# Performance work log

Measured on AMD Instinct MI355X. Metric: run time of the kernel, lower is better.

Reference implementation:

```python
import jax, jax.numpy as jnp
import numpy as np

HEADS = 16
MAX_DIST = 1024

def setup_inputs() -> dict:
    key = jax.random.key(0)
    k1, k2, k3, k4 = jax.random.split(key, 4)
    b, n, dim = 2, 2048, 1024
    x = jax.random.normal(k1, (b, n, dim), dtype=jnp.float32)
    W_qkv = jax.random.normal(k2, (3 * dim, dim), dtype=jnp.float32) * (dim ** -0.5)
    W_out = jax.random.normal(k3, (dim, dim), dtype=jnp.float32) * (dim ** -0.5)
    b_out = jnp.zeros((dim,), dtype=jnp.float32)
    rel_emb = jax.random.normal(k4, (2 * MAX_DIST + 1, HEADS), dtype=jnp.float32) * 0.02
    return {"x": x, "W_qkv": W_qkv, "W_out": W_out, "b_out": b_out, "rel_emb": rel_emb}

def reference(x, W_qkv, W_out, b_out, rel_emb):
    b, n, dim = x.shape
    h = HEADS
    d = dim // h
    scale = d ** -0.5
    qkv = jnp.einsum('bnd,ed->bne', x, W_qkv)  # [b, n, 3*dim]
    q, k, v = jnp.split(qkv, 3, axis=-1)
    def to_heads(t):
        return t.reshape(b, n, h, d).transpose(0, 2, 1, 3)  # b h n d
    q, k, v = to_heads(q), to_heads(k), to_heads(v)
    # relative position bias: [1, h, n, n]
    dist = jnp.arange(n)[None, :] - jnp.arange(n)[:, None]
    idx = jnp.clip(dist, -MAX_DIST, MAX_DIST) + MAX_DIST  # [n, n]
    rel_bias = rel_emb[idx].transpose(2, 0, 1)[None]  # [1, h, n, n]
    scores = jnp.einsum('bhqd,bhkd->bhqk', q, k) * scale + rel_bias
    attn = jax.nn.softmax(scores, axis=-1)
    out = jnp.einsum('bhqk,bhkd->bhqd', attn, v)
    out = out.transpose(0, 2, 1, 3).reshape(b, n, dim)
    return jnp.einsum('bnd,ed->bne', out, W_out) + b_out
```

## Files before the change

### kernel.cpp

```cpp
#include <hip/hip_runtime.h>
#include <hip/hip_bf16.h>

typedef __attribute__((ext_vector_type(8))) short short8;
typedef __attribute__((ext_vector_type(4))) float f32x4;
typedef __attribute__((ext_vector_type(16))) float f32x16;
typedef float f32x4u __attribute__((ext_vector_type(4), aligned(4)));
typedef __attribute__((ext_vector_type(4))) unsigned short u16x4;
typedef __attribute__((ext_vector_type(2))) unsigned int u32x2;
typedef __attribute__((ext_vector_type(4))) unsigned int u32x4;
typedef __hip_bfloat16 bf16;

#define SCALE_Q 0.18033688f

#define GLD_LDS16(g, l) __builtin_amdgcn_global_load_lds(                      \
    (const __attribute__((address_space(1))) void*)(g),                        \
    (__attribute__((address_space(3))) void*)(l), 16, 0, 0)

static __device__ __forceinline__ f32x4 mfma16(short8 a, short8 b, f32x4 c) {
  return __builtin_amdgcn_mfma_f32_16x16x32_bf16(a, b, c, 0, 0, 0);
}
static __device__ __forceinline__ f32x16 mfma32(short8 a, short8 b, f32x16 c) {
  return __builtin_amdgcn_mfma_f32_32x32x16_bf16(a, b, c, 0, 0, 0);
}

static __device__ __forceinline__ unsigned cvtpk(float lo, float hi) {
  unsigned r;
  asm("v_cvt_pk_bf16_f32 %0, %1, %2" : "=v"(r) : "v"(lo), "v"(hi));
  return r;
}

static __device__ __forceinline__ float fexp2(float x) {
  float r;
  asm("v_exp_f32 %0, %1" : "=v"(r) : "v"(x));
  return r;
}

static __device__ __forceinline__ float bf2f(unsigned short u) {
  return __builtin_bit_cast(float, (unsigned)u << 16);
}

#define PLSWAP(a, b) asm("v_permlane32_swap_b32 %0, %1" : "+v"(a), "+v"(b))

__global__ __launch_bounds__(256) void k_pre(
    const float* __restrict__ x, const float* __restrict__ Wqkv,
    const float* __restrict__ Wout, const float* __restrict__ rel,
    bf16* __restrict__ xb, bf16* __restrict__ wqb, bf16* __restrict__ wob,
    float* __restrict__ relpf) {
  int bid = blockIdx.x;
  if (bid < 4096) {
    const float* in;
    bf16* out;
    long i;
    if (bid < 2048) {
      in = x; out = xb; i = (long)bid * 256 + threadIdx.x;
    } else if (bid < 3584) {
      in = Wqkv; out = wqb; i = (long)(bid - 2048) * 256 + threadIdx.x;
    } else {
      in = Wout; out = wob; i = (long)(bid - 3584) * 256 + threadIdx.x;
    }
    f32x4 v0 = *(const f32x4*)(in + i * 8);
    f32x4 v1 = *(const f32x4*)(in + i * 8 + 4);
    u32x4 o;
    o[0] = cvtpk(v0[0], v0[1]);
    o[1] = cvtpk(v0[2], v0[3]);
    o[2] = cvtpk(v1[0], v1[1]);
    o[3] = cvtpk(v1[2], v1[3]);
    *(u32x4*)((unsigned short*)out + i * 8) = o;
  } else {
    int base = (bid - 4096) * 1024 + threadIdx.x;
#pragma unroll
    for (int k = 0; k < 4; ++k) {
      int i = base + k * 256;
      int h = i >> 12, ii = i & 4095;
      int dd = ii - 2047;
      dd = dd < -1024 ? -1024 : (dd > 1024 ? 1024 : dd);
      relpf[i] = rel[(size_t)(dd + 1024) * 16 + h] * 1.44269504f - 16.0f;
    }
  }
}

__global__ __launch_bounds__(256, 3) void k_gemm(
    const bf16* __restrict__ A, const bf16* __restrict__ B,
    int M, int N, int K, int epi,
    bf16* __restrict__ Qb, bf16* __restrict__ Kb, bf16* __restrict__ Vt,
    float* __restrict__ Out, const float* __restrict__ bias) {
  __shared__ bf16 lA[3][4096];
  __shared__ bf16 lB[3][4096];
  const int tid = threadIdx.x, w = tid >> 6, l = tid & 63;
  const int m0 = blockIdx.x * 128, n0 = blockIdx.y * 128;
  const int wrow = (w >> 1) * 64, wcol = (w & 1) * 64;
  const int fr = l & 15, fq = l >> 4;
  f32x4 acc[4][4] = {};
  const int c0 = w * 64 + l, c1 = c0 + 256;
  const bf16* Ag0 = A + (size_t)(m0 + (c0 >> 2)) * K + (c0 & 3) * 8;
  const bf16* Ag1 = A + (size_t)(m0 + (c1 >> 2)) * K + (c1 & 3) * 8;
  const bf16* Bg0 = B + (size_t)(n0 + (c0 >> 2)) * K + (c0 & 3) * 8;
  const bf16* Bg1 = B + (size_t)(n0 + (c1 >> 2)) * K + (c1 & 3) * 8;
  bf16* lA0 = &lA[0][w * 512];
  bf16* lA1 = &lA[0][2048 + w * 512];
  bf16* lB0 = &lB[0][w * 512];
  bf16* lB1 = &lB[0][2048 + w * 512];

#define GSTAGE(T, BI)                                                          \
  do {                                                                         \
    const int ko_ = (T) * 32;                                                  \
    GLD_LDS16(Ag0 + ko_, lA0 + (BI) * 4096);                                   \
    GLD_LDS16(Ag1 + ko_, lA1 + (BI) * 4096);                                   \
    GLD_LDS16(Bg0 + ko_, lB0 + (BI) * 4096);                                   \
    GLD_LDS16(Bg1 + ko_, lB1 + (BI) * 4096);                                   \
  } while (0)

  const int nk = K >> 5;
  GSTAGE(0, 0);
  __builtin_amdgcn_sched_barrier(0);
  GSTAGE(1, 1);
  __builtin_amdgcn_sched_barrier(0);

  int bc_ = 0, bs_ = 2;
  for (int t = 0; t < nk; ++t) {
    asm volatile("s_waitcnt vmcnt(4)" ::: "memory");
    __builtin_amdgcn_s_barrier();
    __builtin_amdgcn_sched_barrier(0);
    int tt = (t + 2 < nk) ? t + 2 : nk - 1;
    GSTAGE(tt, bs_);
    __builtin_amdgcn_sched_barrier(0);
    const bf16* pA = &lA[bc_][0];
    const bf16* pB = &lB[bc_][0];
    short8 af[4], bfv[4];
#pragma unroll
    for (int mi = 0; mi < 4; ++mi)
      af[mi] = *(const short8*)&pA[(wrow + mi * 16 + fr) * 32 + fq * 8];
#pragma unroll
    for (int ni = 0; ni < 4; ++ni)
      bfv[ni] = *(const short8*)&pB[(wcol + ni * 16 + fr) * 32 + fq * 8];
    __builtin_amdgcn_s_setprio(1);
#pragma unroll
    for (int mi = 0; mi < 4; ++mi)
#pragma unroll
      for (int ni = 0; ni < 4; ++ni)
        acc[mi][ni] = mfma16(bfv[ni], af[mi], acc[mi][ni]);
    __builtin_amdgcn_s_setprio(0);
    bc_ = (bc_ == 2) ? 0 : bc_ + 1;
    bs_ = (bs_ == 2) ? 0 : bs_ + 1;
  }
#undef GSTAGE

  if (epi == 0) {
#pragma unroll
    for (int mi = 0; mi < 4; ++mi)
#pragma unroll
      for (int ni = 0; ni < 4; ++ni) {
        int t = m0 + wrow + mi * 16 + fr;
        int e4 = n0 + wcol + ni * 16 + fq * 4;
        int sect = e4 >> 10, eh = (e4 >> 6) & 15, dh = e4 & 63;
        int b = t >> 11, tt = t & 2047;
        f32x4 a = acc[mi][ni];
        if (sect < 2) {
          size_t idx = (((size_t)b * 16 + eh) * 2048 + tt) * 64 + dh;
          float sc = (sect == 0) ? SCALE_Q : 1.f;
          u32x2 ov;
          ov[0] = cvtpk(a[0] * sc, a[1] * sc);
          ov[1] = cvtpk(a[2] * sc, a[3] * sc);
          bf16* dst = (sect == 0) ? Qb : Kb;
          *(u32x2*)(dst + idx) = ov;
        } else {
          size_t vb = ((size_t)((b << 4) + eh) * 64 + dh) * 2048 + tt;
          unsigned p0 = cvtpk(a[0], a[1]);
          unsigned p1 = cvtpk(a[2], a[3]);
          unsigned short* vp = (unsigned short*)Vt;
          vp[vb] = (unsigned short)p0;
          vp[vb + 2048] = (unsigned short)(p0 >> 16);
          vp[vb + 4096] = (unsigned short)p1;
          vp[vb + 6144] = (unsigned short)(p1 >> 16);
        }
      }
  } else {
#pragma unroll
    for (int mi = 0; mi < 4; ++mi)
#pragma unroll
      for (int ni = 0; ni < 4; ++ni) {
        int t = m0 + wrow + mi * 16 + fr;
        int e4 = n0 + wcol + ni * 16 + fq * 4;
        f32x4 bv = *(const f32x4*)(bias + e4);
        f32x4 a = acc[mi][ni];
        f32x4 o = {a[0] + bv[0], a[1] + bv[1], a[2] + bv[2], a[3] + bv[3]};
        *(f32x4*)(Out + (size_t)t * N + e4) = o;
      }
  }
}

__global__ __launch_bounds__(256, 2) void k_attn(
    const bf16* __restrict__ Qb, const bf16* __restrict__ Kb,
    const bf16* __restrict__ Vt, const float* __restrict__ relpf,
    bf16* __restrict__ AO) {
  __shared__ bf16 lK[2][2][4096];
  __shared__ bf16 lV[2][2][4096];

  const int id = blockIdx.x;
  const int xcd = id & 7, j = id >> 3;
  const int bh = xcd * 4 + (j >> 4), qt = j & 15;
  const int h = bh & 15, b = bh >> 4;
  const int tid = threadIdx.x, w = tid >> 6, l = tid & 63;
  const int r32 = l & 31, hl = l >> 5, rs7 = r32 & 7;
  const int qh = w & 1, kvh = w >> 1;
  const int kvb = kvh * 1024;
  const int q0 = qt * 128 + qh * 64;

  const bf16* Kbh = Kb + (size_t)bh * 2048 * 64;
  const bf16* Vbh = Vt + (size_t)bh * 64 * 2048;
  const int pl = tid & 127;
  const bf16* Ksp[4];
  const bf16* Vsp[4];
#pragma unroll
  for (int s = 0; s < 4; ++s) {
    int ck = pl + 128 * s;
    int kr = ck >> 3, kc = (ck & 7) ^ (kr & 7);
    Ksp[s] = Kbh + (size_t)kr * 64 + kc * 8;
    Vsp[s] = Vbh + (size_t)kr * 2048 + kc * 8;
  }

#define STAGE(KT, BI)                                                          \
  do {                                                                         \
    _Pragma("unroll") for (int s_ = 0; s_ < 4; ++s_) {                         \
      int ck_ = pl + 128 * s_;                                                 \
      GLD_LDS16(Ksp[s_] + (size_t)(KT) * 64, &lK[kvh][BI][ck_ * 8]);           \
      GLD_LDS16(Vsp[s_] + (KT), &lV[kvh][BI][ck_ * 8]);                        \
    }                                                                          \
  } while (0)

  const bf16* Qp = Qb + ((size_t)bh * 2048 + q0 + r32) * 64;
  short8 qf0[4], qf1[4];
#pragma unroll
  for (int ks = 0; ks < 4; ++ks) {
    qf0[ks] = *(const short8*)(Qp + ks * 16 + hl * 8);
    qf1[ks] = *(const short8*)(Qp + 32 * 64 + ks * 16 + hl * 8);
  }

  const float* bp0 = relpf + h * 4096 + (2047 + 4 * hl - q0 - r32);
  const float* bp1 = bp0 - 32;

  float ll0 = 0.f, ll1 = 0.f;
  f32x16 oa0 = {}, ob0 = {}, oa1 = {}, ob1 = {};

  STAGE(kvb, 0);
  __builtin_amdgcn_sched_barrier(0);

  int cur = 0;
  for (int t = 0; t < 16; ++t) {
    const int kt = kvb + t * 64;
    asm volatile("s_waitcnt vmcnt(0)" ::: "memory");
    __builtin_amdgcn_s_barrier();
    __builtin_amdgcn_sched_barrier(0);
    f32x16 sa[2], sb[2];
#pragma unroll
    for (int kb = 0; kb < 2; ++kb)
#pragma unroll
      for (int g = 0; g < 4; ++g) {
        f32x4u va = *(const f32x4u*)(bp0 + kt + kb * 32 + 8 * g);
        f32x4u vb = *(const f32x4u*)(bp1 + kt + kb * 32 + 8 * g);
#pragma unroll
        for (int e = 0; e < 4; ++e) {
          sa[kb][g * 4 + e] = va[e];
          sb[kb][g * 4 + e] = vb[e];
        }
      }
    __builtin_amdgcn_sched_barrier(0);
    if (t < 15) STAGE(kt + 64, cur ^ 1);
    __builtin_amdgcn_sched_barrier(0);
    const bf16* lKc = &lK[kvh][cur][0];
    const bf16* lVc = &lV[kvh][cur][0];
    __builtin_amdgcn_s_setprio(1);
#pragma unroll
    for (int kb = 0; kb < 2; ++kb)
#pragma unroll
      for (int ks = 0; ks < 4; ++ks) {
        short8 kf = *(const short8*)&lKc[(kb * 32 + r32) * 64 +
                                         (((2 * ks + hl) ^ rs7) * 8)];
        sa[kb] = mfma32(kf, qf0[ks], sa[kb]);
        sb[kb] = mfma32(kf, qf1[ks], sb[kb]);
      }
    __builtin_amdgcn_s_setprio(0);
    float ra[4] = {0.f, 0.f, 0.f, 0.f}, rb[4] = {0.f, 0.f, 0.f, 0.f};
#pragma unroll
    for (int kb = 0; kb < 2; ++kb)
#pragma unroll
      for (int reg = 0; reg < 16; ++reg) {
        sa[kb][reg] = fexp2(sa[kb][reg]);
        ra[reg & 3] += sa[kb][reg];
        sb[kb][reg] = fexp2(sb[kb][reg]);
        rb[reg & 3] += sb[kb][reg];
      }
    ll0 += (ra[0] + ra[1]) + (ra[2] + ra[3]);
    ll1 += (rb[0] + rb[1]) + (rb[2] + rb[3]);
#pragma unroll
    for (int kb = 0; kb < 2; ++kb) {
#pragma unroll
      for (int kh = 0; kh < 2; ++kh) {
        const int e = kh * 8;
        const int ks = kb * 2 + kh;
        const int cc = ((2 * ks + hl) ^ rs7) * 8;
        unsigned a0 = cvtpk(sa[kb][e + 0], sa[kb][e + 1]);
        unsigned a1 = cvtpk(sa[kb][e + 2], sa[kb][e + 3]);
        unsigned b0 = cvtpk(sa[kb][e + 4], sa[kb][e + 5]);
        unsigned b1 = cvtpk(sa[kb][e + 6], sa[kb][e + 7]);
        PLSWAP(a0, b0);
        PLSWAP(a1, b1);
        u32x4 pw0 = {a0, a1, b0, b1};
        short8 pf0 = __builtin_bit_cast(short8, pw0);
        unsigned c0 = cvtpk(sb[kb][e + 0], sb[kb][e + 1]);
        unsigned c1 = cvtpk(sb[kb][e + 2], sb[kb][e + 3]);
        unsigned d0 = cvtpk(sb[kb][e + 4], sb[kb][e + 5]);
        unsigned d1 = cvtpk(sb[kb][e + 6], sb[kb][e + 7]);
        PLSWAP(c0, d0);
        PLSWAP(c1, d1);
        u32x4 pw1 = {c0, c1, d0, d1};
        short8 pf1 = __builtin_bit_cast(short8, pw1);
        short8 v0 = *(const short8*)&lVc[r32 * 64 + cc];
        short8 v1 = *(const short8*)&lVc[(32 + r32) * 64 + cc];
        __builtin_amdgcn_s_setprio(1);
        oa0 = mfma32(v0, pf0, oa0);
        ob0 = mfma32(v1, pf0, ob0);
        oa1 = mfma32(v0, pf1, oa1);
        ob1 = mfma32(v1, pf1, ob1);
        __builtin_amdgcn_s_setprio(0);
      }
    }
    cur ^= 1;
  }
#undef STAGE

  float l0t = ll0 + __shfl_xor(ll0, 32);
  float l1t = ll1 + __shfl_xor(ll1, 32);
  __syncthreads();
  char* pbase = (qh == 0) ? (char*)&lK[0][0][0] : (char*)&lV[0][0][0];
  float* lf = (float*)(pbase + 64 * 136);
  unsigned* pw = (unsigned*)(pbase + l * 136);
  if (kvh == 1) {
#pragma unroll
    for (int k = 0; k < 8; ++k) {
      pw[k] = cvtpk(oa0[2 * k], oa0[2 * k + 1]);
      pw[8 + k] = cvtpk(ob0[2 * k], ob0[2 * k + 1]);
      pw[16 + k] = cvtpk(oa1[2 * k], oa1[2 * k + 1]);
      pw[24 + k] = cvtpk(ob1[2 * k], ob1[2 * k + 1]);
    }
    if (hl == 0) {
      lf[r32] = l0t;
      lf[32 + r32] = l1t;
    }
  }
  __syncthreads();
  if (kvh == 0) {
    float ls0 = l0t + lf[r32];
    float ls1 = l1t + lf[32 + r32];
#pragma unroll
    for (int k = 0; k < 8; ++k) {
      unsigned u;
      u = pw[k];
      oa0[2 * k] += bf2f((unsigned short)u);
      oa0[2 * k + 1] += bf2f((unsigned short)(u >> 16));
      u = pw[8 + k];
      ob0[2 * k] += bf2f((unsigned short)u);
      ob0[2 * k + 1] += bf2f((unsigned short)(u >> 16));
      u = pw[16 + k];
      oa1[2 * k] += bf2f((unsigned short)u);
      oa1[2 * k + 1] += bf2f((unsigned short)(u >> 16));
      u = pw[24 + k];
      ob1[2 * k] += bf2f((unsigned short)u);
      ob1[2 * k + 1] += bf2f((unsigned short)(u >> 16));
    }
    float rin0 = 1.f / ls0, rin1 = 1.f / ls1;
    bf16* aor = AO + ((size_t)(b * 2048 + q0 + r32)) * 1024 + h * 64 + hl * 4;
    bf16* ao1 = aor + (size_t)32 * 1024;
#pragma unroll
    for (int rg = 0; rg < 4; ++rg) {
      u32x2 ov;
      ov[0] = cvtpk(oa0[4 * rg + 0] * rin0, oa0[4 * rg + 1] * rin0);
      ov[1] = cvtpk(oa0[4 * rg + 2] * rin0, oa0[4 * rg + 3] * rin0);
      *(u32x2*)(aor + rg * 8) = ov;
      ov[0] = cvtpk(ob0[4 * rg + 0] * rin0, ob0[4 * rg + 1] * rin0);
      ov[1] = cvtpk(ob0[4 * rg + 2] * rin0, ob0[4 * rg + 3] * rin0);
      *(u32x2*)(aor + 32 + rg * 8) = ov;
      ov[0] = cvtpk(oa1[4 * rg + 0] * rin1, oa1[4 * rg + 1] * rin1);
      ov[1] = cvtpk(oa1[4 * rg + 2] * rin1, oa1[4 * rg + 3] * rin1);
      *(u32x2*)(ao1 + rg * 8) = ov;
      ov[0] = cvtpk(ob1[4 * rg + 0] * rin1, ob1[4 * rg + 1] * rin1);
      ov[1] = cvtpk(ob1[4 * rg + 2] * rin1, ob1[4 * rg + 3] * rin1);
      *(u32x2*)(ao1 + 32 + rg * 8) = ov;
    }
  }
}

extern "C" void kernel_launch(void* const* d_in, const int* in_sizes, int n_in,
                              void* d_out, int out_size, void* d_ws,
                              size_t ws_size, hipStream_t stream) {
  const float* x = (const float*)d_in[0];
  const float* Wqkv = (const float*)d_in[1];
  const float* Wout = (const float*)d_in[2];
  const float* bout = (const float*)d_in[3];
  const float* rel = (const float*)d_in[4];
  float* out = (float*)d_out;

  char* p = (char*)d_ws;
  bf16* xb  = (bf16*)(p);
  bf16* wqb = (bf16*)(p + (8ull << 20));
  bf16* wob = (bf16*)(p + (14ull << 20));
  bf16* Qb  = (bf16*)(p + (16ull << 20));
  bf16* Kb  = (bf16*)(p + (24ull << 20));
  bf16* Vtr = (bf16*)(p + (32ull << 20));
  bf16* aob = (bf16*)(p + (40ull << 20));
  float* relpf = (float*)(p + (48ull << 20));

  k_pre<<<4160, 256, 0, stream>>>(x, Wqkv, Wout, rel, xb, wqb, wob, relpf);
  k_gemm<<<dim3(32, 24), 256, 0, stream>>>(xb, wqb, 4096, 3072, 1024, 0,
                                           Qb, Kb, Vtr, nullptr, nullptr);
  k_attn<<<512, 256, 0, stream>>>(Qb, Kb, Vtr, relpf, aob);
  k_gemm<<<dim3(32, 8), 256, 0, stream>>>(aob, wob, 4096, 1024, 1024, 1,
                                          nullptr, nullptr, nullptr, out, bout);
}
```

Before: 119.0 us.

## Swizzle GEMM LDS layout and use narrower tiles for output projection

Applies an XOR swizzle to the 16-byte chunk index in the LDS tiles of the QKV GEMM, in both the global-to-LDS load addresses and the fragment reads, to reduce LDS bank conflicts. Adds a dedicated output-projection GEMM with 128x64 tiles, which doubles the grid from 256 to 512 blocks so more CUs are busy on the 4096x1024 problem. The cost is lower per-block reuse of A and a second, near-duplicate kernel to maintain.

```diff
diff --git a/kernel.cpp b/kernel.cpp
--- a/kernel.cpp
+++ b/kernel.cpp
@@ -92,10 +92,11 @@
   const int fr = l & 15, fq = l >> 4;
   f32x4 acc[4][4] = {};
   const int c0 = w * 64 + l, c1 = c0 + 256;
-  const bf16* Ag0 = A + (size_t)(m0 + (c0 >> 2)) * K + (c0 & 3) * 8;
-  const bf16* Ag1 = A + (size_t)(m0 + (c1 >> 2)) * K + (c1 & 3) * 8;
-  const bf16* Bg0 = B + (size_t)(n0 + (c0 >> 2)) * K + (c0 & 3) * 8;
-  const bf16* Bg1 = B + (size_t)(n0 + (c1 >> 2)) * K + (c1 & 3) * 8;
+  const int r0c = c0 >> 2, r1c = c1 >> 2;
+  const bf16* Ag0 = A + (size_t)(m0 + r0c) * K + ((c0 & 3) ^ (r0c & 3)) * 8;
+  const bf16* Ag1 = A + (size_t)(m0 + r1c) * K + ((c1 & 3) ^ (r1c & 3)) * 8;
+  const bf16* Bg0 = B + (size_t)(n0 + r0c) * K + ((c0 & 3) ^ (r0c & 3)) * 8;
+  const bf16* Bg1 = B + (size_t)(n0 + r1c) * K + ((c1 & 3) ^ (r1c & 3)) * 8;
   bf16* lA0 = &lA[0][w * 512];
   bf16* lA1 = &lA[0][2048 + w * 512];
   bf16* lB0 = &lB[0][w * 512];
@@ -128,11 +129,15 @@
     const bf16* pB = &lB[bc_][0];
     short8 af[4], bfv[4];
 #pragma unroll
-    for (int mi = 0; mi < 4; ++mi)
-      af[mi] = *(const short8*)&pA[(wrow + mi * 16 + fr) * 32 + fq * 8];
-#pragma unroll
-    for (int ni = 0; ni < 4; ++ni)
-      bfv[ni] = *(const short8*)&pB[(wcol + ni * 16 + fr) * 32 + fq * 8];
+    for (int mi = 0; mi < 4; ++mi) {
+      int ra = wrow + mi * 16 + fr;
+      af[mi] = *(const short8*)&pA[ra * 32 + ((fq ^ (ra & 3)) * 8)];
+    }
+#pragma unroll
+    for (int ni = 0; ni < 4; ++ni) {
+      int rb = wcol + ni * 16 + fr;
+      bfv[ni] = *(const short8*)&pB[rb * 32 + ((fq ^ (rb & 3)) * 8)];
+    }
     __builtin_amdgcn_s_setprio(1);
 #pragma unroll
     for (int mi = 0; mi < 4; ++mi)
@@ -187,6 +192,83 @@
         *(f32x4*)(Out + (size_t)t * N + e4) = o;
       }
   }
+}
+
+__global__ __launch_bounds__(256, 3) void k_gemm2(
+    const bf16* __restrict__ A, const bf16* __restrict__ B,
+    float* __restrict__ Out, const float* __restrict__ bias) {
+  __shared__ bf16 lA[3][4096];
+  __shared__ bf16 lB[3][2048];
+  const int K = 1024, N = 1024;
+  const int tid = threadIdx.x, w = tid >> 6, l = tid & 63;
+  const int m0 = blockIdx.x * 128, n0 = blockIdx.y * 64;
+  const int wrow = (w >> 1) * 64, wcol = (w & 1) * 32;
+  const int fr = l & 15, fq = l >> 4;
+  f32x4 acc[4][2] = {};
+  const int a0r = tid >> 2, a1r = (tid + 256) >> 2;
+  const bf16* Ag0 = A + (size_t)(m0 + a0r) * K + (((tid & 3) ^ (a0r & 3)) * 8);
+  const bf16* Ag1 = A + (size_t)(m0 + a1r) * K +
+                    ((((tid + 256) & 3) ^ (a1r & 3)) * 8);
+  const bf16* Bg0 = B + (size_t)(n0 + a0r) * K + (((tid & 3) ^ (a0r & 3)) * 8);
+
+#define G2STAGE(T, BI)                                                         \
+  do {                                                                         \
+    const int ko_ = (T) * 32;                                                  \
+    GLD_LDS16(Ag0 + ko_, &lA[BI][tid * 8]);                                    \
+    GLD_LDS16(Ag1 + ko_, &lA[BI][(tid + 256) * 8]);                            \
+    GLD_LDS16(Bg0 + ko_, &lB[BI][tid * 8]);                                    \
+  } while (0)
+
+  const int nk = K >> 5;
+  G2STAGE(0, 0);
+  __builtin_amdgcn_sched_barrier(0);
+  G2STAGE(1, 1);
+  __builtin_amdgcn_sched_barrier(0);
+
+  int bc_ = 0, bs_ = 2;
+  for (int t = 0; t < nk; ++t) {
+    asm volatile("s_waitcnt vmcnt(3)" ::: "memory");
+    __builtin_amdgcn_s_barrier();
+    __builtin_amdgcn_sched_barrier(0);
+    int tt = (t + 2 < nk) ? t + 2 : nk - 1;
+    G2STAGE(tt, bs_);
+    __builtin_amdgcn_sched_barrier(0);
+    const bf16* pA = &lA[bc_][0];
+    const bf16* pB = &lB[bc_][0];
+    short8 af[4], bfv[2];
+#pragma unroll
+    for (int mi = 0; mi < 4; ++mi) {
+      int ra = wrow + mi * 16 + fr;
+      af[mi] = *(const short8*)&pA[ra * 32 + ((fq ^ (ra & 3)) * 8)];
+    }
+#pragma unroll
+    for (int ni = 0; ni < 2; ++ni) {
+      int rb = wcol + ni * 16 + fr;
+      bfv[ni] = *(const short8*)&pB[rb * 32 + ((fq ^ (rb & 3)) * 8)];
+    }
+    __builtin_amdgcn_s_setprio(1);
+#pragma unroll
+    for (int mi = 0; mi < 4; ++mi)
+#pragma unroll
+      for (int ni = 0; ni < 2; ++ni)
+        acc[mi][ni] = mfma16(bfv[ni], af[mi], acc[mi][ni]);
+    __builtin_amdgcn_s_setprio(0);
+    bc_ = (bc_ == 2) ? 0 : bc_ + 1;
+    bs_ = (bs_ == 2) ? 0 : bs_ + 1;
+  }
+#undef G2STAGE
+
+#pragma unroll
+  for (int mi = 0; mi < 4; ++mi)
+#pragma unroll
+    for (int ni = 0; ni < 2; ++ni) {
+      int t = m0 + wrow + mi * 16 + fr;
+      int e4 = n0 + wcol + ni * 16 + fq * 4;
+      f32x4 bv = *(const f32x4*)(bias + e4);
+      f32x4 a = acc[mi][ni];
+      f32x4 o = {a[0] + bv[0], a[1] + bv[1], a[2] + bv[2], a[3] + bv[3]};
+      *(f32x4*)(Out + (size_t)t * N + e4) = o;
+    }
 }
 
 __global__ __launch_bounds__(256, 2) void k_attn(
@@ -414,6 +496,5 @@
   k_gemm<<<dim3(32, 24), 256, 0, stream>>>(xb, wqb, 4096, 3072, 1024, 0,
                                            Qb, Kb, Vtr, nullptr, nullptr);
   k_attn<<<512, 256, 0, stream>>>(Qb, Kb, Vtr, relpf, aob);
-  k_gemm<<<dim3(32, 8), 256, 0, stream>>>(aob, wob, 4096, 1024, 1024, 1,
-                                          nullptr, nullptr, nullptr, out, bout);
-}
+  k_gemm2<<<dim3(32, 16), 256, 0, stream>>>(aob, wob, out, bout);
+}
```

Measured after the change: 115.8 us. 1.03x faster.
